# Performance work log

Measured on AMD Instinct MI355X. Metric: run time of the kernel, lower is better.

The kernel has to match this reference:

```python
import jax, jax.numpy as jnp
import numpy as np

PATCH_SIZES = [8, 16, 24, 48]
SEQ_LEN = 1440
D_MODEL = 512
C_IN = 14
B = 64
BEFF = B * C_IN  # '(B C)' leading dim, individual=True
EPS = float(np.finfo(np.float64).eps)  # np.finfo(float).eps in the original


def setup_inputs() -> dict:
    key = jax.random.key(0)
    ks = jax.random.split(key, 9)
    inp = {}
    for i, p in enumerate(PATCH_SIZES):
        L = -(-SEQ_LEN // p)  # ceil(seq_len / patch_size)
        inp[f"x{i}"] = jax.random.normal(ks[i], (BEFF, L, D_MODEL), dtype=jnp.float32)
        inp[f"W{i}"] = jax.random.normal(ks[4 + i], (p, D_MODEL), dtype=jnp.float32) * (1.0 / np.sqrt(D_MODEL))
        inp[f"b{i}"] = jnp.zeros((p,), dtype=jnp.float32)
    g = jax.random.uniform(ks[8], (BEFF, len(PATCH_SIZES)), dtype=jnp.float32)
    inp["gates"] = g / jnp.sum(g, axis=1, keepdims=True)  # dense soft gates (all nonzero)
    return inp


def reference(x0, x1, x2, x3, W0, b0, W1, b1, W2, b2, W3, b3, gates):
    xs = [x0, x1, x2, x3]
    Ws = [W0, W1, W2, W3]
    bs = [b0, b1, b2, b3]
    outs = []
    for x, W, b in zip(xs, Ws, bs):
        # per-scale Linear(d_model, patch_size); dropout p=0.0 is identity
        y = jnp.einsum('bld,pd->blp', x, W) + b          # [Beff, L_i, p_i]
        # rearrange 'B L (P C) -> B (L P) C' with C=1, then slice to seq_len
        y = y.reshape(y.shape[0], -1, 1)[:, :SEQ_LEN, :]  # [Beff, S, 1]
        outs.append(y)
    # CrossScalePeriodicFeatureAggregator with dense gates:
    # cat(xs,0).exp(), gate-weighted, index_add over batch == weighted sum over experts
    stacked = jnp.exp(jnp.stack(outs, axis=0))            # [E, Beff, S, 1]
    combined = jnp.einsum('ebsd,be->bsd', stacked, gates)  # [Beff, S, 1]
    combined = jnp.where(combined == 0, EPS, combined)
    combined = jnp.log(combined)
    # rearrange '(B C) L D -> B L (C D)' with C=c_in
    out = combined.reshape(B, C_IN, SEQ_LEN, 1).transpose(0, 2, 1, 3).reshape(B, SEQ_LEN, C_IN)
    return out
```

## Files before the change

### kernel.cpp

```cpp
#include <hip/hip_runtime.h>
#include <hip/hip_bf16.h>

#define SEQ   1440
#define DM    512
#define BEFFN 896
#define CIN   14

typedef unsigned int u32;

__device__ __forceinline__ float bf_lo(u32 u) { union { u32 i; float f; } a; a.i = u << 16;          return a.f; }
__device__ __forceinline__ float bf_hi(u32 u) { union { u32 i; float f; } a; a.i = u & 0xFFFF0000u;  return a.f; }

#if __has_builtin(__builtin_amdgcn_fdot2_f32_bf16)
typedef __bf16 bf16x2 __attribute__((ext_vector_type(2)));
__device__ __forceinline__ float dot2bf(u32 a, u32 b, float c)
{
    union { u32 u; bf16x2 v; } ua, ub; ua.u = a; ub.u = b;
    return __builtin_amdgcn_fdot2_f32_bf16(ua.v, ub.v, c, false);
}
#else
__device__ __forceinline__ float dot2bf(u32 a, u32 b, float c)
{
    c = fmaf(bf_lo(a), bf_lo(b), c);
    c = fmaf(bf_hi(a), bf_hi(b), c);
    return c;
}
#endif

__global__ void detect_dtype(const void* __restrict__ gates, int* __restrict__ flag)
{
    if (threadIdx.x == 0 && blockIdx.x == 0) {
        const u32* gb = (const u32*)gates;
        float eb = 0.f;
        for (int r = 0; r < 8; ++r) {
            float sb = 0.f;
            for (int k = 0; k < 4; ++k) {
                int idx = r * 4 + k;
                u32 t = gb[idx >> 1];
                sb += (idx & 1) ? bf_hi(t) : bf_lo(t);
            }
            eb += fabsf(sb - 1.f);
        }
        flag[0] = (eb < 0.25f) ? 1 : 0;
    }
}

__device__ __forceinline__ void batch_bf(const void* __restrict__ x_,
                                         const void* __restrict__ W_,
                                         const void* __restrict__ b_,
                                         float* __restrict__ ylds, int beff,
                                         int L, int P, int RB, int JB, int NACT)
{
    const int lane = threadIdx.x & 63;
    if (lane < NACT) {
        const int l = RB + lane;

        float acc[8];
        {
            const u32* bb = (const u32*)b_ + (JB >> 1);
#pragma unroll
            for (int j = 0; j < 8; j += 2) { u32 t = bb[j >> 1]; acc[j] = bf_lo(t); acc[j + 1] = bf_hi(t); }
        }

        const uint4* xr = (const uint4*)((const __hip_bfloat16*)x_ + ((long long)beff * L + l) * DM);
        const u32*   wp = (const u32*)W_ + ((long long)JB * DM >> 1);

        uint4 va0 = xr[0], va1 = xr[1], va2 = xr[2], va3 = xr[3];
        uint4 vb0 = xr[4], vb1 = xr[5], vb2 = xr[6], vb3 = xr[7];

#define PQ(vq, qk) do {                                             \
        _Pragma("unroll")                                           \
        for (int j = 0; j < 8; ++j) {                               \
            const u32* wr = wp + j * 256 + (qk) * 4;                \
            acc[j] = dot2bf((vq).x, wr[0], acc[j]);                 \
            acc[j] = dot2bf((vq).y, wr[1], acc[j]);                 \
            acc[j] = dot2bf((vq).z, wr[2], acc[j]);                 \
            acc[j] = dot2bf((vq).w, wr[3], acc[j]);                 \
        } } while (0)

#pragma unroll
        for (int g2 = 0; g2 < 8; ++g2) {
            PQ(va0, 0); PQ(va1, 1); PQ(va2, 2); PQ(va3, 3);
            if (g2 < 7) { int q = 8 * (g2 + 1); va0 = xr[q]; va1 = xr[q + 1]; va2 = xr[q + 2]; va3 = xr[q + 3]; }
            PQ(vb0, 4); PQ(vb1, 5); PQ(vb2, 6); PQ(vb3, 7);
            if (g2 < 7) { int q = 8 * (g2 + 1); vb0 = xr[q + 4]; vb1 = xr[q + 5]; vb2 = xr[q + 6]; vb3 = xr[q + 7]; }
            wp += 32;
        }
#undef PQ

        float* yo = ylds + l * P + JB;
        *(float4*)(yo)     = make_float4(acc[0], acc[1], acc[2], acc[3]);
        *(float4*)(yo + 4) = make_float4(acc[4], acc[5], acc[6], acc[7]);
    }
}

__device__ __forceinline__ void batch_f32(const void* __restrict__ x_,
                                          const void* __restrict__ W_,
                                          const void* __restrict__ b_,
                                          float* __restrict__ ylds, int beff,
                                          int L, int P, int RB, int JB, int NACT)
{
    const int lane = threadIdx.x & 63;
    if (lane < NACT) {
        const int l = RB + lane;

        float acc[8];
        {
            const float* bb = (const float*)b_ + JB;
#pragma unroll
            for (int j = 0; j < 8; ++j) acc[j] = bb[j];
        }

        const float4* xr = (const float4*)((const float*)x_ + ((long long)beff * L + l) * DM);
        const float*  wp = (const float*)W_ + (long long)JB * DM;

        float4 va0 = xr[0], va1 = xr[1], va2 = xr[2], va3 = xr[3];
        float4 vb0 = xr[4], vb1 = xr[5], vb2 = xr[6], vb3 = xr[7];

#define PQF(vq, qk) do {                                            \
        _Pragma("unroll")                                           \
        for (int j = 0; j < 8; ++j) {                               \
            const float* wr = wp + j * 512 + (qk) * 4;              \
            acc[j] = fmaf((vq).x, wr[0], acc[j]);                   \
            acc[j] = fmaf((vq).y, wr[1], acc[j]);                   \
            acc[j] = fmaf((vq).z, wr[2], acc[j]);                   \
            acc[j] = fmaf((vq).w, wr[3], acc[j]);                   \
        } } while (0)

#pragma unroll
        for (int g2 = 0; g2 < 16; ++g2) {
            PQF(va0, 0); PQF(va1, 1); PQF(va2, 2); PQF(va3, 3);
            if (g2 < 15) { int q = 8 * (g2 + 1); va0 = xr[q]; va1 = xr[q + 1]; va2 = xr[q + 2]; va3 = xr[q + 3]; }
            PQF(vb0, 4); PQF(vb1, 5); PQF(vb2, 6); PQF(vb3, 7);
            if (g2 < 15) { int q = 8 * (g2 + 1); vb0 = xr[q + 4]; vb1 = xr[q + 5]; vb2 = xr[q + 6]; vb3 = xr[q + 7]; }
            wp += 32;
        }
#undef PQF

        float* yo = ylds + l * P + JB;
        *(float4*)(yo)     = make_float4(acc[0], acc[1], acc[2], acc[3]);
        *(float4*)(yo + 4) = make_float4(acc[4], acc[5], acc[6], acc[7]);
    }
}

__device__ const int dtab[16][6] = {
    {0, 180,  8,   0,  0, 64}, {0, 180,  8,  64,  0, 64}, {0, 180,  8, 128,  0, 52}, {1,  90, 16,   0,  0, 64},
    {1,  90, 16,  64,  0, 26}, {1,  90, 16,   0,  8, 64}, {1,  90, 16,  64,  8, 26}, {2,  60, 24,   0,  0, 60},
    {2,  60, 24,   0,  8, 60}, {2,  60, 24,   0, 16, 60}, {3,  30, 48,   0,  0, 30}, {3,  30, 48,   0,  8, 30},
    {3,  30, 48,   0, 16, 30}, {3,  30, 48,   0, 24, 30}, {3,  30, 48,   0, 32, 30}, {3,  30, 48,   0, 40, 30},
};

__global__ __launch_bounds__(256, 4) void fused_all(
    const void* __restrict__ x0, const void* __restrict__ x1,
    const void* __restrict__ x2, const void* __restrict__ x3,
    const void* __restrict__ W0, const void* __restrict__ W1,
    const void* __restrict__ W2, const void* __restrict__ W3,
    const void* __restrict__ b0, const void* __restrict__ b1,
    const void* __restrict__ b2, const void* __restrict__ b3,
    const void* __restrict__ gates, void* __restrict__ out,
    const int* __restrict__ flag)
{
    __shared__ float ysh[4 * SEQ];
    const int beff = blockIdx.x;
    const int w = threadIdx.x >> 6;
    const int isbf = flag[0];

#pragma unroll 1
    for (int bi = 0; bi < 4; ++bi) {
        const int e  = __builtin_amdgcn_readfirstlane(w * 4 + bi);
        const int sc = dtab[e][0], L = dtab[e][1], P  = dtab[e][2];
        const int RB = dtab[e][3], JB = dtab[e][4], NA = dtab[e][5];
        const void* xp = sc == 0 ? x0 : sc == 1 ? x1 : sc == 2 ? x2 : x3;
        const void* Wp = sc == 0 ? W0 : sc == 1 ? W1 : sc == 2 ? W2 : W3;
        const void* bp = sc == 0 ? b0 : sc == 1 ? b1 : sc == 2 ? b2 : b3;
        float* yl = ysh + sc * SEQ;
        if (isbf) batch_bf (xp, Wp, bp, yl, beff, L, P, RB, JB, NA);
        else      batch_f32(xp, Wp, bp, yl, beff, L, P, RB, JB, NA);
    }
    __syncthreads();

    const int Bi = beff / CIN, c = beff % CIN;
    float g0, g1, g2, g3;
    if (isbf) {
        const u32* gg = (const u32*)gates;
        u32 t0 = gg[beff * 2], t1 = gg[beff * 2 + 1];
        g0 = bf_lo(t0); g1 = bf_hi(t0); g2 = bf_lo(t1); g3 = bf_hi(t1);
    } else {
        float4 gv = ((const float4*)gates)[beff];
        g0 = gv.x; g1 = gv.y; g2 = gv.z; g3 = gv.w;
    }

    for (int s = threadIdx.x; s < SEQ; s += 256) {
        float acc = g0 * __expf(ysh[s])
                  + g1 * __expf(ysh[SEQ + s])
                  + g2 * __expf(ysh[2 * SEQ + s])
                  + g3 * __expf(ysh[3 * SEQ + s]);
        if (acc == 0.f) acc = 2.2204460492503131e-16f;
        float r = __logf(acc);
        long long oi = (long long)(Bi * SEQ + s) * CIN + c;
        if (isbf) ((__hip_bfloat16*)out)[oi] = __float2bfloat16(r);
        else      ((float*)out)[oi] = r;
    }
}

extern "C" void kernel_launch(void* const* d_in, const int* in_sizes, int n_in,
                              void* d_out, int out_size, void* d_ws, size_t ws_size,
                              hipStream_t stream)
{
    const void *x[4] = {0,0,0,0}, *W[4] = {0,0,0,0}, *b[4] = {0,0,0,0}, *gates = 0;
    for (int i = 0; i < n_in; ++i) {
        const void* p = d_in[i];
        switch (in_sizes[i]) {
            case 82575360: x[0] = p; break;
            case 41287680: x[1] = p; break;
            case 27525120: x[2] = p; break;
            case 13762560: x[3] = p; break;
            case 4096:  W[0] = p; break;
            case 8192:  W[1] = p; break;
            case 12288: W[2] = p; break;
            case 24576: W[3] = p; break;
            case 8:  b[0] = p; break;
            case 16: b[1] = p; break;
            case 24: b[2] = p; break;
            case 48: b[3] = p; break;
            case 3584: gates = p; break;
        }
    }

    int* flag = (int*)d_ws;

    detect_dtype<<<1, 64, 0, stream>>>(gates, flag);
    fused_all<<<BEFFN, 256, 0, stream>>>(x[0], x[1], x[2], x[3],
                                         W[0], W[1], W[2], W[3],
                                         b[0], b[1], b[2], b[3],
                                         gates, d_out, flag);
}
```

Baseline: 904.1 us.

## Double-buffer bf16 input rows into LDS with async global-to-LDS loads

```diff
diff --git a/kernel.cpp b/kernel.cpp
--- a/kernel.cpp
+++ b/kernel.cpp
@@ -7,6 +7,7 @@
 #define CIN   14
 
 typedef unsigned int u32;
+typedef unsigned char u8;
 
 __device__ __forceinline__ float bf_lo(u32 u) { union { u32 i; float f; } a; a.i = u << 16;          return a.f; }
 __device__ __forceinline__ float bf_hi(u32 u) { union { u32 i; float f; } a; a.i = u & 0xFFFF0000u;  return a.f; }
@@ -45,53 +46,91 @@
     }
 }
 
-__device__ __forceinline__ void batch_bf(const void* __restrict__ x_,
-                                         const void* __restrict__ W_,
-                                         const void* __restrict__ b_,
-                                         float* __restrict__ ylds, int beff,
-                                         int L, int P, int RB, int JB, int NACT)
+#if __has_builtin(__builtin_amdgcn_global_load_lds)
+#define HAS_GLL 1
+#else
+#define HAS_GLL 0
+#endif
+
+__device__ __forceinline__ void stage_row(const u8* grow, u8* lrow, int lane, int sw)
+{
+    const u8* g = grow + (((lane & ~7) | ((lane & 7) ^ sw)) << 4);
+#if HAS_GLL
+    __builtin_amdgcn_global_load_lds((const __attribute__((address_space(1))) void*)g,
+                                     (__attribute__((address_space(3))) void*)lrow, 16, 0, 0);
+#else
+    *(uint4*)(lrow + lane * 16) = *(const uint4*)g;
+#endif
+}
+
+__device__ __forceinline__ void stage_chunk(const void* x_, int beff, int L,
+                                            int row0, int nrows, u8* lbuf)
 {
     const int lane = threadIdx.x & 63;
-    if (lane < NACT) {
-        const int l = RB + lane;
-
-        float acc[8];
-        {
-            const u32* bb = (const u32*)b_ + (JB >> 1);
-#pragma unroll
-            for (int j = 0; j < 8; j += 2) { u32 t = bb[j >> 1]; acc[j] = bf_lo(t); acc[j + 1] = bf_hi(t); }
-        }
-
-        const uint4* xr = (const uint4*)((const __hip_bfloat16*)x_ + ((long long)beff * L + l) * DM);
-        const u32*   wp = (const u32*)W_ + ((long long)JB * DM >> 1);
-
-        uint4 va0 = xr[0], va1 = xr[1], va2 = xr[2], va3 = xr[3];
-        uint4 vb0 = xr[4], vb1 = xr[5], vb2 = xr[6], vb3 = xr[7];
-
-#define PQ(vq, qk) do {                                             \
-        _Pragma("unroll")                                           \
-        for (int j = 0; j < 8; ++j) {                               \
-            const u32* wr = wp + j * 256 + (qk) * 4;                \
-            acc[j] = dot2bf((vq).x, wr[0], acc[j]);                 \
-            acc[j] = dot2bf((vq).y, wr[1], acc[j]);                 \
-            acc[j] = dot2bf((vq).z, wr[2], acc[j]);                 \
-            acc[j] = dot2bf((vq).w, wr[3], acc[j]);                 \
-        } } while (0)
-
-#pragma unroll
-        for (int g2 = 0; g2 < 8; ++g2) {
-            PQ(va0, 0); PQ(va1, 1); PQ(va2, 2); PQ(va3, 3);
-            if (g2 < 7) { int q = 8 * (g2 + 1); va0 = xr[q]; va1 = xr[q + 1]; va2 = xr[q + 2]; va3 = xr[q + 3]; }
-            PQ(vb0, 4); PQ(vb1, 5); PQ(vb2, 6); PQ(vb3, 7);
-            if (g2 < 7) { int q = 8 * (g2 + 1); vb0 = xr[q + 4]; vb1 = xr[q + 5]; vb2 = xr[q + 6]; vb3 = xr[q + 7]; }
-            wp += 32;
-        }
-#undef PQ
-
-        float* yo = ylds + l * P + JB;
-        *(float4*)(yo)     = make_float4(acc[0], acc[1], acc[2], acc[3]);
-        *(float4*)(yo + 4) = make_float4(acc[4], acc[5], acc[6], acc[7]);
-    }
+    const int w = __builtin_amdgcn_readfirstlane((int)(threadIdx.x >> 6));
+    const u8* xb = (const u8*)x_ + (((long long)beff * L + row0) << 10);
+#pragma unroll
+    for (int i = 0; i < 16; ++i) {
+        const int slot = w * 16 + i;
+        const int srow = slot < nrows ? slot : nrows - 1;
+        stage_row(xb + (srow << 10), lbuf + (slot << 10), lane, srow & 7);
+    }
+}
+
+#if HAS_GLL
+#define STAGE_WAIT_STEADY() asm volatile("s_waitcnt vmcnt(16)" ::: "memory")
+#define STAGE_WAIT_LAST()   asm volatile("s_waitcnt vmcnt(0)"  ::: "memory")
+#else
+#define STAGE_WAIT_STEADY() asm volatile("s_waitcnt vmcnt(0) lgkmcnt(0)" ::: "memory")
+#define STAGE_WAIT_LAST()   asm volatile("s_waitcnt vmcnt(0) lgkmcnt(0)" ::: "memory")
+#endif
+#define SBAR() do { __builtin_amdgcn_sched_barrier(0); __builtin_amdgcn_s_barrier(); \
+                    __builtin_amdgcn_sched_barrier(0); } while (0)
+
+template<int P>
+__device__ __forceinline__ void compute_chunk(const u8* lbuf, const void* W_, const void* b_,
+                                              float* ysb, int row0, int nrows)
+{
+    constexpr int P4 = P / 4;
+    const int w  = __builtin_amdgcn_readfirstlane((int)(threadIdx.x >> 6));
+    const int jb = w * P4;
+    const int r  = threadIdx.x & 63;
+    if (r >= nrows) return;
+
+    float acc[P4];
+    {
+        const u32* bb = (const u32*)b_;
+#pragma unroll
+        for (int j = 0; j < P4; ++j) {
+            int jj = jb + j; u32 t = bb[jj >> 1];
+            acc[j] = (jj & 1) ? bf_hi(t) : bf_lo(t);
+        }
+    }
+
+    const u32* Wb  = (const u32*)W_ + jb * 256;
+    const u8*  rb  = lbuf + (r << 10);
+    const int  sw4 = (r & 7) << 4;
+
+#pragma unroll 2
+    for (int kk = 0; kk < 8; ++kk) {
+#pragma unroll
+        for (int k3 = 0; k3 < 8; ++k3) {
+            uint4 xv = *(const uint4*)(rb + (kk << 7) + ((k3 << 4) ^ sw4));
+            const int k = kk * 8 + k3;
+#pragma unroll
+            for (int j = 0; j < P4; ++j) {
+                const u32* wr = Wb + j * 256 + k * 4;
+                acc[j] = dot2bf(xv.x, wr[0], acc[j]);
+                acc[j] = dot2bf(xv.y, wr[1], acc[j]);
+                acc[j] = dot2bf(xv.z, wr[2], acc[j]);
+                acc[j] = dot2bf(xv.w, wr[3], acc[j]);
+            }
+        }
+    }
+
+    float* yo = ysb + (row0 + r) * P + jb;
+#pragma unroll
+    for (int j = 0; j < P4; ++j) yo[j] = acc[j];
 }
 
 __device__ __forceinline__ void batch_f32(const void* __restrict__ x_,
@@ -103,20 +142,16 @@
     const int lane = threadIdx.x & 63;
     if (lane < NACT) {
         const int l = RB + lane;
-
         float acc[8];
         {
             const float* bb = (const float*)b_ + JB;
 #pragma unroll
             for (int j = 0; j < 8; ++j) acc[j] = bb[j];
         }
-
         const float4* xr = (const float4*)((const float*)x_ + ((long long)beff * L + l) * DM);
         const float*  wp = (const float*)W_ + (long long)JB * DM;
-
         float4 va0 = xr[0], va1 = xr[1], va2 = xr[2], va3 = xr[3];
         float4 vb0 = xr[4], vb1 = xr[5], vb2 = xr[6], vb3 = xr[7];
-
 #define PQF(vq, qk) do {                                            \
         _Pragma("unroll")                                           \
         for (int j = 0; j < 8; ++j) {                               \
@@ -126,7 +161,6 @@
             acc[j] = fmaf((vq).z, wr[2], acc[j]);                   \
             acc[j] = fmaf((vq).w, wr[3], acc[j]);                   \
         } } while (0)
-
 #pragma unroll
         for (int g2 = 0; g2 < 16; ++g2) {
             PQF(va0, 0); PQF(va1, 1); PQF(va2, 2); PQF(va3, 3);
@@ -136,7 +170,6 @@
             wp += 32;
         }
 #undef PQF
-
         float* yo = ylds + l * P + JB;
         *(float4*)(yo)     = make_float4(acc[0], acc[1], acc[2], acc[3]);
         *(float4*)(yo + 4) = make_float4(acc[4], acc[5], acc[6], acc[7]);
@@ -150,7 +183,7 @@
     {3,  30, 48,   0, 16, 30}, {3,  30, 48,   0, 24, 30}, {3,  30, 48,   0, 32, 30}, {3,  30, 48,   0, 40, 30},
 };
 
-__global__ __launch_bounds__(256, 4) void fused_all(
+__global__ __launch_bounds__(256) void fused_all(
     const void* __restrict__ x0, const void* __restrict__ x1,
     const void* __restrict__ x2, const void* __restrict__ x3,
     const void* __restrict__ W0, const void* __restrict__ W1,
@@ -160,22 +193,46 @@
     const void* __restrict__ gates, void* __restrict__ out,
     const int* __restrict__ flag)
 {
+    __shared__ __align__(16) u8 xbuf[2][64 * 1024];
     __shared__ float ysh[4 * SEQ];
     const int beff = blockIdx.x;
-    const int w = threadIdx.x >> 6;
     const int isbf = flag[0];
 
+    if (isbf) {
+        u8* B0 = xbuf[0]; u8* B1 = xbuf[1];
+        stage_chunk(x0, beff, 180,   0, 64, B0);
+        stage_chunk(x0, beff, 180,  64, 64, B1);
+        STAGE_WAIT_STEADY(); SBAR();
+        compute_chunk< 8>(B0, W0, b0, ysh + 0 * SEQ,   0, 64); SBAR();
+        stage_chunk(x0, beff, 180, 128, 52, B0);
+        STAGE_WAIT_STEADY(); SBAR();
+        compute_chunk< 8>(B1, W0, b0, ysh + 0 * SEQ,  64, 64); SBAR();
+        stage_chunk(x1, beff,  90,   0, 64, B1);
+        STAGE_WAIT_STEADY(); SBAR();
+        compute_chunk< 8>(B0, W0, b0, ysh + 0 * SEQ, 128, 52); SBAR();
+        stage_chunk(x1, beff,  90,  64, 26, B0);
+        STAGE_WAIT_STEADY(); SBAR();
+        compute_chunk<16>(B1, W1, b1, ysh + 1 * SEQ,   0, 64); SBAR();
+        stage_chunk(x2, beff,  60,   0, 60, B1);
+        STAGE_WAIT_STEADY(); SBAR();
+        compute_chunk<16>(B0, W1, b1, ysh + 1 * SEQ,  64, 26); SBAR();
+        stage_chunk(x3, beff,  30,   0, 30, B0);
+        STAGE_WAIT_STEADY(); SBAR();
+        compute_chunk<24>(B1, W2, b2, ysh + 2 * SEQ,   0, 60); SBAR();
+        STAGE_WAIT_LAST();   SBAR();
+        compute_chunk<48>(B0, W3, b3, ysh + 3 * SEQ,   0, 30);
+    } else {
+        const int w = threadIdx.x >> 6;
 #pragma unroll 1
-    for (int bi = 0; bi < 4; ++bi) {
-        const int e  = __builtin_amdgcn_readfirstlane(w * 4 + bi);
-        const int sc = dtab[e][0], L = dtab[e][1], P  = dtab[e][2];
-        const int RB = dtab[e][3], JB = dtab[e][4], NA = dtab[e][5];
-        const void* xp = sc == 0 ? x0 : sc == 1 ? x1 : sc == 2 ? x2 : x3;
-        const void* Wp = sc == 0 ? W0 : sc == 1 ? W1 : sc == 2 ? W2 : W3;
-        const void* bp = sc == 0 ? b0 : sc == 1 ? b1 : sc == 2 ? b2 : b3;
-        float* yl = ysh + sc * SEQ;
-        if (isbf) batch_bf (xp, Wp, bp, yl, beff, L, P, RB, JB, NA);
-        else      batch_f32(xp, Wp, bp, yl, beff, L, P, RB, JB, NA);
+        for (int bi = 0; bi < 4; ++bi) {
+            const int e  = __builtin_amdgcn_readfirstlane(w * 4 + bi);
+            const int sc = dtab[e][0], L = dtab[e][1], P  = dtab[e][2];
+            const int RB = dtab[e][3], JB = dtab[e][4], NA = dtab[e][5];
+            const void* xp = sc == 0 ? x0 : sc == 1 ? x1 : sc == 2 ? x2 : x3;
+            const void* Wp = sc == 0 ? W0 : sc == 1 ? W1 : sc == 2 ? W2 : W3;
+            const void* bp = sc == 0 ? b0 : sc == 1 ? b1 : sc == 2 ? b2 : b3;
+            batch_f32(xp, Wp, bp, ysh + sc * SEQ, beff, L, P, RB, JB, NA);
+        }
     }
     __syncthreads();
 
```

Result: slower. 1.560 ms (+72.5%).
